# Kernel optimization log

Hardware: AMD Instinct MI355X
Metric: run time of the kernel (lower is better)

Reference implementation:

```python
import jax, jax.numpy as jnp
import numpy as np

B, G, D, L, F = 64, 1024, 256, 2, 1024  # batch, graph_size, embed_dim, n_layers, ffn hidden
NEG = -30.0  # mask fill value when evaluate=False (training path)


def _uniform(key, shape, fan):
    stdv = 1.0 / np.sqrt(fan)
    return jax.random.uniform(key, shape, jnp.float32, -stdv, stdv)


def setup_inputs() -> dict:
    key = jax.random.key(0)
    ks = jax.random.split(key, 12)
    x = jax.random.normal(ks[0], (B, G, D), jnp.float32)
    mask = jax.random.randint(ks[1], (B, G), 0, 2, jnp.int32)  # 1 = attention blocked
    # weights stored as [in, out] (transposed vs torch Linear); same math.
    Wq = _uniform(ks[2], (L, D, D), D)
    Wk = _uniform(ks[3], (L, D, D), D)
    Wv = _uniform(ks[4], (L, D, D), D)
    Wo = _uniform(ks[5], (L, D, D), D)
    bo = _uniform(ks[6], (L, D), D)
    Wf1 = _uniform(ks[7], (L, D, F), D)
    bf1 = _uniform(ks[8], (L, F), F)
    Wf2 = _uniform(ks[9], (L, F, D), F)
    bf2 = _uniform(ks[10], (L, D), D)
    return {"x": x, "mask": mask, "Wq": Wq, "Wk": Wk, "Wv": Wv,
            "Wo": Wo, "bo": bo, "Wf1": Wf1, "bf1": bf1, "Wf2": Wf2, "bf2": bf2}


def reference(x, mask, Wq, Wk, Wv, Wo, bo, Wf1, bf1, Wf2, bf2):
    # GraphAttentionEncoder with n_heads=1 (key_dim = val_dim = embed_dim).
    m = mask.astype(bool)[:, None, :]            # [B,1,G] -> broadcast over query dim
    norm = 1.0 / jnp.sqrt(jnp.asarray(D, x.dtype))
    h = x
    for l in range(L):
        # --- MultiHeadAttention with residual (SkipConnection) ---
        q = h @ Wq[l]                            # [B,G,D]
        k = h @ Wk[l]
        v = h @ Wv[l]
        c = norm * jnp.einsum('bqd,bkd->bqk', q, k)   # [B,G,G]
        c = jnp.where(m, NEG, c)                 # masked fill (-30, evaluate=False)
        a = jax.nn.softmax(c, axis=-1)
        a = jnp.where(m, 0.0, a)                 # post-softmax zeroing of masked weights
        heads = jnp.einsum('bqk,bkd->bqd', a, v)
        h = h + heads @ Wo[l] + bo[l]
        # --- feed-forward with residual (SkipConnection_Linear) ---
        h = h + jax.nn.relu(h @ Wf1[l] + bf1[l]) @ Wf2[l] + bf2[l]
    return h, h.mean(axis=1)
```

## Files before the change

kernel.cpp:

```cpp
#include <hip/hip_runtime.h>
#include <hip/hip_bf16.h>

#define Bdim 64
#define Gdim 1024
#define Ddim 256
#define Fdim 1024

typedef short s8v __attribute__((ext_vector_type(8)));
typedef short s4v __attribute__((ext_vector_type(4)));
typedef float f4v __attribute__((ext_vector_type(4)));

__device__ __forceinline__ float bf2f(short s){
  return __uint_as_float(((unsigned)(unsigned short)s) << 16);
}
__device__ __forceinline__ short f2bf(float f){
  unsigned u = __float_as_uint(f);
  u = u + 0x7fffu + ((u >> 16) & 1u);
  return (short)(u >> 16);
}
__device__ __forceinline__ s8v ld8(const short* p){ return *(const s8v*)p; }

#define MFMA_BF16(a,b,c) __builtin_amdgcn_mfma_f32_16x16x32_bf16((a),(b),(c),0,0,0)

#define GLDS16(gp, lp) __builtin_amdgcn_global_load_lds( \
    (const __attribute__((address_space(1))) void*)(gp), \
    (__attribute__((address_space(3))) void*)(lp), 16, 0, 0)

__global__ __launch_bounds__(256) void detect_dtype(const unsigned* __restrict__ x,
                                                    int* __restrict__ flag){
  __shared__ int cnt[256];
  int c = 0;
  #pragma unroll
  for (int j=0;j<4;j++){
    unsigned u = x[threadIdx.x*4 + j];
    int e = (u >> 7) & 0xFF;
    c += (e >= 100 && e <= 140) ? 1 : 0;
  }
  cnt[threadIdx.x] = c;
  __syncthreads();
  if (threadIdx.x == 0){
    int s = 0;
    for (int i=0;i<256;i++) s += cnt[i];
    flag[0] = (s >= 512) ? 0 : 1;
  }
}

__global__ void diag_ws(void* o, float v, const int* __restrict__ flag){
  if (threadIdx.x == 0){
    if (flag[0]){ ((float*)o)[0] = v; ((float*)o)[16777216] = v; }
    else        { ((short*)o)[0] = f2bf(v); ((short*)o)[16777216] = f2bf(v); }
  }
}

__global__ __launch_bounds__(256) void cast_in(const void* __restrict__ x,
                                               float* __restrict__ h32,
                                               const int* __restrict__ flag){
  size_t i = ((size_t)blockIdx.x * 256 + threadIdx.x) * 8;
  if (flag[0]){
    const float* xf = (const float*)x;
    #pragma unroll
    for (int j=0;j<8;j++) h32[i+j] = xf[i+j];
  } else {
    s8v v = ld8((const short*)x + i);
    #pragma unroll
    for (int j=0;j<8;j++) h32[i+j] = bf2f(v[j]);
  }
}

__global__ __launch_bounds__(256) void transpose_w(const void* __restrict__ src,
                                                   short* __restrict__ dh, int R, int C,
                                                   const int* __restrict__ flag,
                                                   int dzs, int dbase){
  __shared__ short th[32][33];
  int fl = flag[0];
  size_t soff = (size_t)blockIdx.z * R * C;
  size_t doff = (size_t)dbase + (size_t)blockIdx.z * dzs;
  int c0 = blockIdx.x*32, r0 = blockIdx.y*32;
  int tx = threadIdx.x, ty = threadIdx.y;
  #pragma unroll
  for (int i=ty;i<32;i+=8){
    size_t idx = soff + (size_t)(r0+i)*C + (c0+tx);
    float w = fl ? ((const float*)src)[idx] : bf2f(((const short*)src)[idx]);
    th[i][tx] = f2bf(w);
  }
  __syncthreads();
  #pragma unroll
  for (int i=ty;i<32;i+=8)
    dh[doff + (size_t)(c0+i)*R + (r0+tx)] = th[tx][i];
}

__global__ __launch_bounds__(256) void bias_prep(const void* __restrict__ bo,
                                                 const void* __restrict__ bf1,
                                                 const void* __restrict__ bf2,
                                                 float* __restrict__ biasf,
                                                 const int* __restrict__ flag){
  int fl = flag[0];
  int i = blockIdx.x*256 + threadIdx.x;
  const void* src; int idx;
  if (i < 512){ src = bo; idx = i; }
  else if (i < 2560){ src = bf1; idx = i - 512; }
  else { src = bf2; idx = i - 2560; }
  biasf[i] = fl ? ((const float*)src)[idx] : bf2f(((const short*)src)[idx]);
}

template<int AM, int EPI>
__global__ __launch_bounds__(256) void gemm_t(
    const void* __restrict__ Ap, const short* __restrict__ Bh,
    const float* __restrict__ bias, float* __restrict__ hout,
    short* __restrict__ outb, int N, int K, int lda, int ldb, int Mrows)
{
  constexpr int AT = (AM==2) ? 2 : 1;
  __shared__ short As[AT*128*40];
  __shared__ short Bs[128*40];
  short* Asl = As + 128*40;
  const int tid = threadIdx.x;
  const int lane = tid & 63, wave = tid >> 6;
  const int quad = lane >> 4, l16 = lane & 15;
  const int m0 = blockIdx.x * 128, n0 = blockIdx.y * 128;
  const int wr = wave >> 1, wc = wave & 1;
  f4v acc[4][4];
  #pragma unroll
  for (int i=0;i<4;i++)
    #pragma unroll
    for (int j=0;j<4;j++) acc[i][j] = f4v{0.f,0.f,0.f,0.f};

  for (int k0 = 0; k0 < K; k0 += 32){
    __syncthreads();
    #pragma unroll
    for (int i=0;i<2;i++){
      int v = tid + i*256;
      int r = v >> 2, c8 = (v & 3) * 8;
      if (AM == 0){
        *(s8v*)(&As[r*40 + c8]) = ld8((const short*)Ap + (size_t)(m0 + r)*lda + k0 + c8);
      } else {
        const float* af = (const float*)Ap + (size_t)(m0 + r)*lda + k0 + c8;
        float4 f0 = *(const float4*)af;
        float4 f1 = *(const float4*)(af + 4);
        float fv[8] = {f0.x,f0.y,f0.z,f0.w,f1.x,f1.y,f1.z,f1.w};
        s8v hi, lo;
        #pragma unroll
        for (int j=0;j<8;j++) hi[j] = f2bf(fv[j]);
        *(s8v*)(&As[r*40 + c8]) = hi;
        if (AM == 2){
          #pragma unroll
          for (int j=0;j<8;j++) lo[j] = f2bf(fv[j] - bf2f(hi[j]));
          *(s8v*)(&Asl[r*40 + c8]) = lo;
        }
      }
      *(s8v*)(&Bs[r*40 + c8]) = ld8(Bh + (size_t)(n0 + r)*ldb + k0 + c8);
    }
    __syncthreads();
    s8v ah[4], al[4], bh[4];
    #pragma unroll
    for (int t=0;t<4;t++){
      ah[t] = ld8(&As[(wr*64 + t*16 + l16)*40 + quad*8]);
      bh[t] = ld8(&Bs[(wc*64 + t*16 + l16)*40 + quad*8]);
      if (AM == 2) al[t] = ld8(&Asl[(wr*64 + t*16 + l16)*40 + quad*8]);
    }
    #pragma unroll
    for (int ti=0;ti<4;ti++)
      #pragma unroll
      for (int tj=0;tj<4;tj++){
        acc[ti][tj] = MFMA_BF16(ah[ti], bh[tj], acc[ti][tj]);
        if (AM == 2) acc[ti][tj] = MFMA_BF16(al[ti], bh[tj], acc[ti][tj]);
      }
  }
  #pragma unroll
  for (int tj=0;tj<4;tj++){
    int col = n0 + wc*64 + tj*16 + l16;
    float bs = (EPI==1 || EPI==4) ? (bias ? bias[col] : 0.f) : 0.f;
    #pragma unroll
    for (int ti=0;ti<4;ti++){
      #pragma unroll
      for (int r=0;r<4;r++){
        int row = m0 + wr*64 + ti*16 + quad*4 + r;
        float v = acc[ti][tj][r];
        if (EPI == 0){
          outb[(size_t)row * N + col] = f2bf(v);
        } else if (EPI == 1){
          v += bs; v = v > 0.f ? v : 0.f;
          outb[(size_t)row * N + col] = f2bf(v);
        } else if (EPI == 4){
          size_t idx = (size_t)row * N + col;
          hout[idx] += v + bs;
        } else {
          int sec = col >> 8, c = col & 255;
          if (sec == 0)      outb[(size_t)row*256 + c] = f2bf(v);
          else if (sec == 1) (outb + (size_t)Mrows*256)[(size_t)row*256 + c] = f2bf(v);
          else {
            int bb = row >> 10, g = row & 1023;
            (outb + (size_t)2*Mrows*256)[(size_t)bb*262144 + (size_t)c*1024 + g] = f2bf(v);
          }
        }
      }
    }
  }
}

__global__ __launch_bounds__(512, 2) void flash_attn(
    const short* __restrict__ Q, const short* __restrict__ Kmat,
    const short* __restrict__ Vt, const int* __restrict__ mask,
    short* __restrict__ H)
{
  __shared__ short Ks[2][64*256];
  __shared__ short Vs[2][256*64];
  __shared__ short Ps[8][16*72];
  const int tid = threadIdx.x;
  const int lane = tid & 63, wave = tid >> 6;
  const int quad = lane >> 4, l16 = lane & 15;
  const int bid = blockIdx.x;
  const int b  = (bid & 7) + ((bid >> 6) << 3);
  const int qt = (bid >> 3) & 7;
  const short* Qb  = Q    + (size_t)b*Gdim*Ddim;
  const short* Kb  = Kmat + (size_t)b*Gdim*Ddim;
  const short* Vtb = Vt   + (size_t)b*Ddim*Gdim;
  const int qbase = qt*128 + wave*16;

  auto stage = [&](int buf, int k0){
    #pragma unroll
    for (int i=0;i<4;i++){
      int idx = i*512 + tid;
      int r = idx >> 5, g = idx & 31;
      GLDS16(Kb + (size_t)(k0 + r)*Ddim + ((g ^ (r & 7)) << 3), &Ks[buf][idx*8]);
    }
    #pragma unroll
    for (int i=0;i<4;i++){
      int idx = i*512 + tid;
      int d = idx >> 3, g = idx & 7;
      GLDS16(Vtb + (size_t)d*Gdim + k0 + ((g ^ (d & 7)) << 3), &Vs[buf][idx*8]);
    }
  };

  s8v qf[8];
  #pragma unroll
  for (int s=0;s<8;s++)
    qf[s] = ld8(Qb + (size_t)(qbase + l16)*Ddim + s*32 + quad*8);
  float mrow = -1e9f, lsum = 0.f;
  f4v O[16];
  #pragma unroll
  for (int t=0;t<16;t++) O[t] = f4v{0.f,0.f,0.f,0.f};
  short* Pw = Ps[wave];

  stage(0, 0);
  __syncthreads();
  int cur = 0;
  for (int kt=0; kt<16; kt++){
    const int k0 = kt*64;
    if (kt < 15) stage(cur^1, k0 + 64);
    int mv = mask[b*Gdim + k0 + lane];
    f4v sc[4];
    #pragma unroll
    for (int tj=0;tj<4;tj++) sc[tj] = f4v{0.f,0.f,0.f,0.f};
    const short* Kc = &Ks[cur][0];
    __builtin_amdgcn_s_setprio(1);
    #pragma unroll
    for (int st=0; st<8; st++){
      #pragma unroll
      for (int tj=0;tj<4;tj++){
        int row = tj*16 + l16;
        s8v kb = ld8(Kc + row*256 + (((st*4 + quad) ^ (row & 7)) << 3));
        sc[tj] = MFMA_BF16(kb, qf[st], sc[tj]);
      }
    }
    __builtin_amdgcn_s_setprio(0);
    unsigned long long mb = __ballot(mv != 0);
    float pm = -1e9f;
    #pragma unroll
    for (int tj=0;tj<4;tj++){
      unsigned mb4 = (unsigned)(mb >> (tj*16 + quad*4)) & 15u;
      #pragma unroll
      for (int r=0;r<4;r++){
        float v = sc[tj][r] * 0.0625f;
        if ((mb4 >> r) & 1u) v = -30.f;
        sc[tj][r] = v;
        pm = fmaxf(pm, v);
      }
    }
    pm = fmaxf(pm, __shfl_xor(pm, 16));
    pm = fmaxf(pm, __shfl_xor(pm, 32));
    if (!__all(pm <= mrow + 8.f)){
      float mn = fmaxf(mrow, pm);
      float al = __expf(mrow - mn);
      mrow = mn;
      lsum *= al;
      float alr[4];
      #pragma unroll
      for (int r=0;r<4;r++) alr[r] = __shfl(al, quad*4 + r);
      #pragma unroll
      for (int t=0;t<16;t++)
        #pragma unroll
        for (int r=0;r<4;r++) O[t][r] *= alr[r];
    }
    float ps = 0.f;
    #pragma unroll
    for (int tj=0;tj<4;tj++){
      unsigned mb4 = (unsigned)(mb >> (tj*16 + quad*4)) & 15u;
      s4v pk;
      #pragma unroll
      for (int r=0;r<4;r++){
        float e = __expf(sc[tj][r] - mrow);
        ps += e;
        pk[r] = ((mb4 >> r) & 1u) ? (short)0 : f2bf(e);
      }
      *(s4v*)(&Pw[l16*72 + tj*16 + quad*4]) = pk;
    }
    lsum += ps;
    asm volatile("s_waitcnt lgkmcnt(0)" ::: "memory");
    __builtin_amdgcn_sched_barrier(0);
    const short* Vc = &Vs[cur][0];
    __builtin_amdgcn_s_setprio(1);
    #pragma unroll
    for (int st=0; st<2; st++){
      s8v pa = ld8(&Pw[l16*72 + st*32 + quad*8]);
      #pragma unroll
      for (int tt=0; tt<16; tt++){
        int d = tt*16 + l16;
        s8v vb = ld8(Vc + d*64 + (((st*4 + quad) ^ (d & 7)) << 3));
        O[tt] = MFMA_BF16(pa, vb, O[tt]);
      }
    }
    __builtin_amdgcn_s_setprio(0);
    __syncthreads();
    cur ^= 1;
  }
  float s = lsum;
  s += __shfl_xor(s, 16);
  s += __shfl_xor(s, 32);
  float dnr[4];
  #pragma unroll
  for (int r=0;r<4;r++) dnr[r] = fmaxf(__shfl(s, quad*4 + r), 1e-30f);
  #pragma unroll
  for (int t=0;t<16;t++){
    #pragma unroll
    for (int r=0;r<4;r++){
      int row = qbase + quad*4 + r;
      int col = t*16 + l16;
      H[((size_t)b*Gdim + row)*Ddim + col] = f2bf(O[t][r] / dnr[r]);
    }
  }
}

__global__ __launch_bounds__(256) void mean_partial(const float* __restrict__ h32,
                                                    float* __restrict__ part){
  int b = blockIdx.x, c = blockIdx.y, d = threadIdx.x;
  float s = 0.f;
  for (int g = c*64; g < c*64 + 64; g++)
    s += h32[((size_t)b*Gdim + g)*Ddim + d];
  part[(b*16 + c)*Ddim + d] = s;
}
__global__ __launch_bounds__(256) void mean_final_dyn(const float* __restrict__ part,
                                                      void* __restrict__ out,
                                                      const int* __restrict__ flag){
  int i = blockIdx.x*256 + threadIdx.x;
  int b = i >> 8, d = i & 255;
  float s = 0.f;
  #pragma unroll
  for (int c=0;c<16;c++) s += part[(b*16 + c)*Ddim + d];
  s *= (1.f/1024.f);
  if (flag[0]) ((float*)out)[16777216 + i] = s;
  else         ((short*)out)[16777216 + i] = f2bf(s);
}
__global__ __launch_bounds__(256) void store_h(const float* __restrict__ h32,
                                               void* __restrict__ out,
                                               const int* __restrict__ flag){
  size_t i = (size_t)blockIdx.x*256 + threadIdx.x;
  if (flag[0]) ((float*)out)[i] = h32[i];
  else         ((short*)out)[i] = f2bf(h32[i]);
}

extern "C" void kernel_launch(void* const* d_in, const int* in_sizes, int n_in,
                              void* d_out, int out_size, void* d_ws, size_t ws_size,
                              hipStream_t stream)
{
  const void* xs  = d_in[0];
  const int*  mask= (const int*)d_in[1];
  const void* Wq  = d_in[2];
  const void* Wk  = d_in[3];
  const void* Wv  = d_in[4];
  const void* Wo  = d_in[5];
  const void* bo  = d_in[6];
  const void* Wf1 = d_in[7];
  const void* bf1 = d_in[8];
  const void* Wf2 = d_in[9];
  const void* bf2 = d_in[10];

  const size_t W_ALL = 786432 + 262144 + 1048576 + 1048576 + 12288;
  const size_t BASE  = 256 + 67108864;
  int CB;
  if      (ws_size >= BASE + 134217728ull + W_ALL) CB = 64;
  else if (ws_size >= BASE +  67108864ull + W_ALL) CB = 32;
  else if (ws_size >= BASE +  33554432ull + W_ALL) CB = 16;
  else CB = 0;

  char* p = (char*)d_ws;
  int* flag = (int*)p; p += 256;
  detect_dtype<<<1, 256, 0, stream>>>((const unsigned*)xs, flag);
  if (CB == 0){
    diag_ws<<<1, 64, 0, stream>>>(d_out, 2000.f + (float)(ws_size >> 20), flag);
    return;
  }
  const int M = CB * 1024, nch = 64 / CB;
  float* h32 = (float*)p; p += 67108864;
  char* arena = p;        p += (size_t)CB * 2097152;
  short* WqkvT = (short*)p; p += 786432;
  short* WoT   = (short*)p; p += 262144;
  short* Wf1T  = (short*)p; p += 1048576;
  short* Wf2T  = (short*)p; p += 1048576;
  float* biasf = (float*)p; p += 12288;
  float* part  = (float*)arena;

  short* Qc  = (short*)arena;
  short* Kc  = Qc + (size_t)M*256;
  short* Vtc = Qc + (size_t)2*M*256;
  short* Hc  = Qc + (size_t)3*M*256;
  short* Tc  = Qc;

  cast_in<<<8192, 256, 0, stream>>>(xs, h32, flag);
  dim3 tb(32,8);
  transpose_w<<<dim3(8,8,2),  tb, 0, stream>>>(Wq,  WqkvT, 256, 256,  flag, 196608, 0);
  transpose_w<<<dim3(8,8,2),  tb, 0, stream>>>(Wk,  WqkvT, 256, 256,  flag, 196608, 65536);
  transpose_w<<<dim3(8,8,2),  tb, 0, stream>>>(Wv,  WqkvT, 256, 256,  flag, 196608, 131072);
  transpose_w<<<dim3(8,8,2),  tb, 0, stream>>>(Wo,  WoT,   256, 256,  flag, 65536, 0);
  transpose_w<<<dim3(32,8,2), tb, 0, stream>>>(Wf1, Wf1T,  256, 1024, flag, 262144, 0);
  transpose_w<<<dim3(8,32,2), tb, 0, stream>>>(Wf2, Wf2T,  1024, 256, flag, 262144, 0);
  bias_prep<<<12, 256, 0, stream>>>(bo, bf1, bf2, biasf, flag);

  for (int c=0; c<nch; c++){
    float* hc = h32 + (size_t)c*M*256;
    const int* mc = mask + (size_t)c*M;
    for (int l=0; l<2; l++){
      gemm_t<1,5><<<dim3(M/128,6), 256, 0, stream>>>(hc, WqkvT + l*196608, nullptr,
                                                     nullptr, Qc, 768, 256, 256, 256, M);
      flash_attn<<<dim3(8*CB), 512, 0, stream>>>(Qc, Kc, Vtc, mc, Hc);
      gemm_t<0,4><<<dim3(M/128,2), 256, 0, stream>>>(Hc, WoT + l*65536, biasf + l*256,
                                                     hc, nullptr, 256, 256, 256, 256, M);
      gemm_t<2,1><<<dim3(M/128,8), 256, 0, stream>>>(hc, Wf1T + l*262144, biasf + 512 + l*1024,
                                                     nullptr, Tc, 1024, 256, 256, 256, M);
      gemm_t<0,4><<<dim3(M/128,2), 256, 0, stream>>>(Tc, Wf2T + l*262144, biasf + 2560 + l*256,
                                                     hc, nullptr, 256, 1024, 1024, 1024, M);
    }
  }
  mean_partial<<<dim3(64,16), 256, 0, stream>>>(h32, part);
  store_h<<<65536, 256, 0, stream>>>(h32, d_out, flag);
  mean_final_dyn<<<64, 256, 0, stream>>>(part, d_out, flag);
}
```

Before: 1.176 ms.

## Rewrite flash attention with 32x32 MFMA and split-KV waves within block

The attention kernel switches from 16x16x32 to 32x32x16 bf16 MFMA tiles, with each wave now owning 32 query rows. The block's 8 waves split into two KV halves of 512 keys each, processed in 32-key steps. The two partial softmax states are merged at the end through LDS scratch. The aim is fewer LDS fragment loads per FLOP and better MFMA efficiency, at the cost of more registers, a final cross-wave reduction, and shorter K-loop steps with more per-step overhead.

New measurement: 1.283 ms. +9.1%, slower.

```diff
diff --git a/kernel.cpp b/kernel.cpp
--- a/kernel.cpp
+++ b/kernel.cpp
@@ -9,6 +9,7 @@
 typedef short s8v __attribute__((ext_vector_type(8)));
 typedef short s4v __attribute__((ext_vector_type(4)));
 typedef float f4v __attribute__((ext_vector_type(4)));
+typedef float f16f __attribute__((ext_vector_type(16)));
 
 __device__ __forceinline__ float bf2f(short s){
   return __uint_as_float(((unsigned)(unsigned short)s) << 16);
@@ -21,6 +22,7 @@
 __device__ __forceinline__ s8v ld8(const short* p){ return *(const s8v*)p; }
 
 #define MFMA_BF16(a,b,c) __builtin_amdgcn_mfma_f32_16x16x32_bf16((a),(b),(c),0,0,0)
+#define MFMA32(a,b,c)    __builtin_amdgcn_mfma_f32_32x32x16_bf16((a),(b),(c),0,0,0)
 
 #define GLDS16(gp, lp) __builtin_amdgcn_global_load_lds( \
     (const __attribute__((address_space(1))) void*)(gp), \
@@ -202,140 +204,161 @@
     const short* __restrict__ Vt, const int* __restrict__ mask,
     short* __restrict__ H)
 {
-  __shared__ short Ks[2][64*256];
-  __shared__ short Vs[2][256*64];
-  __shared__ short Ps[8][16*72];
+  __shared__ short Ks[2][2][8192];
+  __shared__ short Vs[2][2][8192];
+  __shared__ short Ps[8][1280];
   const int tid = threadIdx.x;
   const int lane = tid & 63, wave = tid >> 6;
-  const int quad = lane >> 4, l16 = lane & 15;
+  const int hi = lane >> 5, l32 = lane & 31;
+  const int g = wave & 3, kvh = wave >> 2;
   const int bid = blockIdx.x;
   const int b  = (bid & 7) + ((bid >> 6) << 3);
   const int qt = (bid >> 3) & 7;
   const short* Qb  = Q    + (size_t)b*Gdim*Ddim;
   const short* Kb  = Kmat + (size_t)b*Gdim*Ddim;
   const short* Vtb = Vt   + (size_t)b*Ddim*Gdim;
-  const int qbase = qt*128 + wave*16;
-
-  auto stage = [&](int buf, int k0){
-    #pragma unroll
-    for (int i=0;i<4;i++){
-      int idx = i*512 + tid;
-      int r = idx >> 5, g = idx & 31;
-      GLDS16(Kb + (size_t)(k0 + r)*Ddim + ((g ^ (r & 7)) << 3), &Ks[buf][idx*8]);
-    }
-    #pragma unroll
-    for (int i=0;i<4;i++){
-      int idx = i*512 + tid;
-      int d = idx >> 3, g = idx & 7;
-      GLDS16(Vtb + (size_t)d*Gdim + k0 + ((g ^ (d & 7)) << 3), &Vs[buf][idx*8]);
+  const int qbase = qt*128 + g*32;
+
+  int kco[2], vco[2], cdst[2];
+  #pragma unroll
+  for (int i=0;i<2;i++){
+    int idx = i*512 + tid;
+    int r = idx >> 5, gg = idx & 31;
+    kco[i] = r*256 + ((gg ^ (r & 7)) << 3);
+    int d = idx >> 2, gv = idx & 3;
+    vco[i] = d*1024 + ((gv ^ (d & 3)) << 3);
+    cdst[i] = idx*8;
+  }
+  auto stage = [&](int buf, int it){
+    const short* k0p = Kb + (size_t)(it*32)*256;
+    const short* k1p = k0p + 512*256;
+    #pragma unroll
+    for (int i=0;i<2;i++){
+      GLDS16(k0p + kco[i], &Ks[0][buf][cdst[i]]);
+      GLDS16(k1p + kco[i], &Ks[1][buf][cdst[i]]);
+      GLDS16(Vtb + vco[i] + it*32,       &Vs[0][buf][cdst[i]]);
+      GLDS16(Vtb + vco[i] + it*32 + 512, &Vs[1][buf][cdst[i]]);
     }
   };
 
-  s8v qf[8];
-  #pragma unroll
-  for (int s=0;s<8;s++)
-    qf[s] = ld8(Qb + (size_t)(qbase + l16)*Ddim + s*32 + quad*8);
+  s8v qf[16];
+  const short* Qrow = Qb + (size_t)(qbase + l32)*Ddim + hi*8;
+  #pragma unroll
+  for (int s=0;s<16;s++) qf[s] = ld8(Qrow + s*16);
   float mrow = -1e9f, lsum = 0.f;
-  f4v O[16];
-  #pragma unroll
-  for (int t=0;t<16;t++) O[t] = f4v{0.f,0.f,0.f,0.f};
+  f16f O[8];
+  #pragma unroll
+  for (int dg=0;dg<8;dg++)
+    #pragma unroll
+    for (int r=0;r<16;r++) O[dg][r] = 0.f;
   short* Pw = Ps[wave];
 
   stage(0, 0);
   __syncthreads();
   int cur = 0;
-  for (int kt=0; kt<16; kt++){
-    const int k0 = kt*64;
-    if (kt < 15) stage(cur^1, k0 + 64);
-    int mv = mask[b*Gdim + k0 + lane];
-    f4v sc[4];
-    #pragma unroll
-    for (int tj=0;tj<4;tj++) sc[tj] = f4v{0.f,0.f,0.f,0.f};
-    const short* Kc = &Ks[cur][0];
+  const short* KsS = &Ks[kvh][0][0];
+  const short* VsS = &Vs[kvh][0][0];
+  const int mbase = b*Gdim + kvh*512;
+  for (int it=0; it<16; it++){
+    if (it < 15) stage(cur^1, it+1);
+    int mv = mask[mbase + it*32 + l32];
+    f16f sc;
+    #pragma unroll
+    for (int r=0;r<16;r++) sc[r] = 0.f;
+    const short* Kst = KsS + cur*8192;
+    const int krow = l32*256, ksw = l32 & 7;
     __builtin_amdgcn_s_setprio(1);
     #pragma unroll
-    for (int st=0; st<8; st++){
-      #pragma unroll
-      for (int tj=0;tj<4;tj++){
-        int row = tj*16 + l16;
-        s8v kb = ld8(Kc + row*256 + (((st*4 + quad) ^ (row & 7)) << 3));
-        sc[tj] = MFMA_BF16(kb, qf[st], sc[tj]);
-      }
+    for (int s=0;s<16;s++){
+      s8v kf = ld8(Kst + krow + (((s*2 + hi) ^ ksw) << 3));
+      sc = MFMA32(kf, qf[s], sc);
     }
     __builtin_amdgcn_s_setprio(0);
-    unsigned long long mb = __ballot(mv != 0);
+    unsigned mb = (unsigned)__ballot(mv != 0);
     float pm = -1e9f;
     #pragma unroll
-    for (int tj=0;tj<4;tj++){
-      unsigned mb4 = (unsigned)(mb >> (tj*16 + quad*4)) & 15u;
-      #pragma unroll
-      for (int r=0;r<4;r++){
-        float v = sc[tj][r] * 0.0625f;
-        if ((mb4 >> r) & 1u) v = -30.f;
-        sc[tj][r] = v;
-        pm = fmaxf(pm, v);
-      }
-    }
-    pm = fmaxf(pm, __shfl_xor(pm, 16));
+    for (int r=0;r<16;r++){
+      int kk = (r & 3) + 8*(r >> 2) + 4*hi;
+      float v = sc[r] * 0.0625f;
+      if ((mb >> kk) & 1u) v = -30.f;
+      sc[r] = v;
+      pm = fmaxf(pm, v);
+    }
     pm = fmaxf(pm, __shfl_xor(pm, 32));
     if (!__all(pm <= mrow + 8.f)){
       float mn = fmaxf(mrow, pm);
       float al = __expf(mrow - mn);
-      mrow = mn;
-      lsum *= al;
-      float alr[4];
-      #pragma unroll
-      for (int r=0;r<4;r++) alr[r] = __shfl(al, quad*4 + r);
-      #pragma unroll
-      for (int t=0;t<16;t++)
+      mrow = mn; lsum *= al;
+      #pragma unroll
+      for (int r=0;r<16;r++){
+        float alr = __shfl(al, (r & 3) + 8*(r >> 2) + 4*hi);
         #pragma unroll
-        for (int r=0;r<4;r++) O[t][r] *= alr[r];
+        for (int dg=0;dg<8;dg++) O[dg][r] *= alr;
+      }
     }
     float ps = 0.f;
     #pragma unroll
-    for (int tj=0;tj<4;tj++){
-      unsigned mb4 = (unsigned)(mb >> (tj*16 + quad*4)) & 15u;
+    for (int rq=0; rq<4; rq++){
       s4v pk;
       #pragma unroll
-      for (int r=0;r<4;r++){
-        float e = __expf(sc[tj][r] - mrow);
+      for (int j=0;j<4;j++){
+        int r = rq*4 + j;
+        int kk = j + 8*rq + 4*hi;
+        float e = __expf(sc[r] - mrow);
         ps += e;
-        pk[r] = ((mb4 >> r) & 1u) ? (short)0 : f2bf(e);
-      }
-      *(s4v*)(&Pw[l16*72 + tj*16 + quad*4]) = pk;
+        pk[j] = ((mb >> kk) & 1u) ? (short)0 : f2bf(e);
+      }
+      *(s4v*)(&Pw[l32*40 + rq*8 + hi*4]) = pk;
     }
     lsum += ps;
     asm volatile("s_waitcnt lgkmcnt(0)" ::: "memory");
     __builtin_amdgcn_sched_barrier(0);
-    const short* Vc = &Vs[cur][0];
+    const short* Vst = VsS + cur*8192;
     __builtin_amdgcn_s_setprio(1);
     #pragma unroll
-    for (int st=0; st<2; st++){
-      s8v pa = ld8(&Pw[l16*72 + st*32 + quad*8]);
-      #pragma unroll
-      for (int tt=0; tt<16; tt++){
-        int d = tt*16 + l16;
-        s8v vb = ld8(Vc + d*64 + (((st*4 + quad) ^ (d & 7)) << 3));
-        O[tt] = MFMA_BF16(pa, vb, O[tt]);
+    for (int c=0;c<2;c++){
+      s8v pa = ld8(&Pw[l32*40 + c*16 + hi*8]);
+      #pragma unroll
+      for (int dg=0;dg<8;dg++){
+        int d = dg*32 + l32;
+        s8v vb = ld8(Vst + d*32 + ((((c*2 + hi) ^ (d & 3))) << 3));
+        O[dg] = MFMA32(pa, vb, O[dg]);
       }
     }
     __builtin_amdgcn_s_setprio(0);
     __syncthreads();
     cur ^= 1;
   }
-  float s = lsum;
-  s += __shfl_xor(s, 16);
-  s += __shfl_xor(s, 32);
-  float dnr[4];
-  #pragma unroll
-  for (int r=0;r<4;r++) dnr[r] = fmaxf(__shfl(s, quad*4 + r), 1e-30f);
-  #pragma unroll
-  for (int t=0;t<16;t++){
-    #pragma unroll
-    for (int r=0;r<4;r++){
-      int row = qbase + quad*4 + r;
-      int col = t*16 + l16;
-      H[((size_t)b*Gdim + row)*Ddim + col] = f2bf(O[t][r] / dnr[r]);
+  float dn = lsum + __shfl_xor(lsum, 32);
+  float* scr = (g < 2) ? ((float*)&Ks[0][0][0] + g*8192)
+                       : ((float*)&Vs[0][0][0] + (g - 2)*8192);
+  float* ml = (float*)&Ps[0][0];
+  if (kvh == 1){
+    #pragma unroll
+    for (int dg=0;dg<8;dg++)
+      #pragma unroll
+      for (int r=0;r<16;r++)
+        scr[(dg*16 + r)*64 + lane] = O[dg][r];
+    if (hi == 0){ ml[g*32 + l32] = mrow; ml[128 + g*32 + l32] = dn; }
+  }
+  __syncthreads();
+  if (kvh == 0){
+    float mh = ml[g*32 + l32], dh = ml[128 + g*32 + l32];
+    float m12 = fmaxf(mrow, mh);
+    float el = __expf(mrow - m12), eh = __expf(mh - m12);
+    float dnf = dn*el + dh*eh;
+    #pragma unroll
+    for (int r=0;r<16;r++){
+      int cr = (r & 3) + 8*(r >> 2) + 4*hi;
+      float elr = __shfl(el, cr);
+      float ehr = __shfl(eh, cr);
+      float dnr = fmaxf(__shfl(dnf, cr), 1e-30f);
+      int row = qbase + cr;
+      #pragma unroll
+      for (int dg=0;dg<8;dg++){
+        float ov = O[dg][r]*elr + scr[(dg*16 + r)*64 + lane]*ehr;
+        H[((size_t)b*Gdim + row)*Ddim + dg*32 + l32] = f2bf(ov / dnr);
+      }
     }
   }
 }
```

## Split KV sequence across wave halves with 32-row query tiles per wave

Applied to the files above, without the earlier changes.

Each wave now handles 32 query rows, so every K and V fragment loaded from LDS feeds two MFMAs instead of one. The eight waves split into two groups that each cover half of the key sequence, in 32-key chunks, and at the end the partial softmax states are merged through shared memory. The aim is to cut LDS read traffic per MFMA and shorten the serial KV loop. In exchange the accumulator register count doubles, which may pressure occupancy at launch bounds (512,2), and a cross-wave merge step is added.

Measured after the change: 1.295 ms. +10.2%, slower.

```diff
diff --git a/kernel.cpp b/kernel.cpp
--- a/kernel.cpp
+++ b/kernel.cpp
@@ -202,140 +202,182 @@
     const short* __restrict__ Vt, const int* __restrict__ mask,
     short* __restrict__ H)
 {
-  __shared__ short Ks[2][64*256];
-  __shared__ short Vs[2][256*64];
-  __shared__ short Ps[8][16*72];
+  __shared__ short Ks[2][2][32*256];
+  __shared__ short Vs[2][2][256*32];
+  __shared__ short Ps[8][32*40];
   const int tid = threadIdx.x;
   const int lane = tid & 63, wave = tid >> 6;
   const int quad = lane >> 4, l16 = lane & 15;
+  const int g = wave & 3, kvh = wave >> 2;
   const int bid = blockIdx.x;
   const int b  = (bid & 7) + ((bid >> 6) << 3);
   const int qt = (bid >> 3) & 7;
   const short* Qb  = Q    + (size_t)b*Gdim*Ddim;
   const short* Kb  = Kmat + (size_t)b*Gdim*Ddim;
   const short* Vtb = Vt   + (size_t)b*Ddim*Gdim;
-  const int qbase = qt*128 + wave*16;
-
-  auto stage = [&](int buf, int k0){
-    #pragma unroll
-    for (int i=0;i<4;i++){
+  const int qbase = qt*128 + g*32;
+
+  auto stage = [&](int buf, int it){
+    #pragma unroll
+    for (int i=0;i<2;i++){
       int idx = i*512 + tid;
-      int r = idx >> 5, g = idx & 31;
-      GLDS16(Kb + (size_t)(k0 + r)*Ddim + ((g ^ (r & 7)) << 3), &Ks[buf][idx*8]);
-    }
-    #pragma unroll
-    for (int i=0;i<4;i++){
-      int idx = i*512 + tid;
-      int d = idx >> 3, g = idx & 7;
-      GLDS16(Vtb + (size_t)d*Gdim + k0 + ((g ^ (d & 7)) << 3), &Vs[buf][idx*8]);
+      int r = idx >> 5, gg = idx & 31;
+      int ko = r*256 + ((gg ^ (r & 7)) << 3);
+      GLDS16(Kb + (size_t)(it*32)*256 + ko,        &Ks[0][buf][idx*8]);
+      GLDS16(Kb + (size_t)(512 + it*32)*256 + ko,  &Ks[1][buf][idx*8]);
+      int d = idx >> 2, gv = idx & 3;
+      int vo = d*1024 + ((gv ^ (d & 3)) << 3);
+      GLDS16(Vtb + vo + it*32,        &Vs[0][buf][idx*8]);
+      GLDS16(Vtb + vo + it*32 + 512,  &Vs[1][buf][idx*8]);
     }
   };
 
-  s8v qf[8];
-  #pragma unroll
-  for (int s=0;s<8;s++)
-    qf[s] = ld8(Qb + (size_t)(qbase + l16)*Ddim + s*32 + quad*8);
-  float mrow = -1e9f, lsum = 0.f;
-  f4v O[16];
-  #pragma unroll
-  for (int t=0;t<16;t++) O[t] = f4v{0.f,0.f,0.f,0.f};
+  s8v qf0[8], qf1[8];
+  {
+    const short* Qr0 = Qb + (size_t)(qbase + l16)*Ddim + quad*8;
+    #pragma unroll
+    for (int s=0;s<8;s++){
+      qf0[s] = ld8(Qr0 + s*32);
+      qf1[s] = ld8(Qr0 + 16*Ddim + s*32);
+    }
+  }
+  float mrow0 = -1e9f, mrow1 = -1e9f, lsum0 = 0.f, lsum1 = 0.f;
+  f4v O0[16], O1[16];
+  #pragma unroll
+  for (int t=0;t<16;t++){ O0[t]=f4v{0.f,0.f,0.f,0.f}; O1[t]=f4v{0.f,0.f,0.f,0.f}; }
   short* Pw = Ps[wave];
+  const int ksw = l16 & 7, vsw = quad ^ (l16 & 3);
 
   stage(0, 0);
   __syncthreads();
   int cur = 0;
-  for (int kt=0; kt<16; kt++){
-    const int k0 = kt*64;
-    if (kt < 15) stage(cur^1, k0 + 64);
-    int mv = mask[b*Gdim + k0 + lane];
-    f4v sc[4];
-    #pragma unroll
-    for (int tj=0;tj<4;tj++) sc[tj] = f4v{0.f,0.f,0.f,0.f};
-    const short* Kc = &Ks[cur][0];
+  const int mbase = b*Gdim + kvh*512;
+  for (int it=0; it<16; it++){
+    if (it < 15) stage(cur^1, it+1);
+    int mv = mask[mbase + it*32 + (lane & 31)];
+    f4v sc0[2], sc1[2];
+    sc0[0]=sc0[1]=f4v{0.f,0.f,0.f,0.f};
+    sc1[0]=sc1[1]=f4v{0.f,0.f,0.f,0.f};
+    const short* Kst = &Ks[kvh][cur][0];
     __builtin_amdgcn_s_setprio(1);
     #pragma unroll
     for (int st=0; st<8; st++){
-      #pragma unroll
-      for (int tj=0;tj<4;tj++){
-        int row = tj*16 + l16;
-        s8v kb = ld8(Kc + row*256 + (((st*4 + quad) ^ (row & 7)) << 3));
-        sc[tj] = MFMA_BF16(kb, qf[st], sc[tj]);
-      }
+      int off = (((st*4 + quad) ^ ksw) << 3);
+      s8v kfa = ld8(Kst + l16*256 + off);
+      s8v kfb = ld8(Kst + (16 + l16)*256 + off);
+      sc0[0] = MFMA_BF16(kfa, qf0[st], sc0[0]);
+      sc0[1] = MFMA_BF16(kfb, qf0[st], sc0[1]);
+      sc1[0] = MFMA_BF16(kfa, qf1[st], sc1[0]);
+      sc1[1] = MFMA_BF16(kfb, qf1[st], sc1[1]);
     }
     __builtin_amdgcn_s_setprio(0);
-    unsigned long long mb = __ballot(mv != 0);
-    float pm = -1e9f;
-    #pragma unroll
-    for (int tj=0;tj<4;tj++){
-      unsigned mb4 = (unsigned)(mb >> (tj*16 + quad*4)) & 15u;
-      #pragma unroll
-      for (int r=0;r<4;r++){
-        float v = sc[tj][r] * 0.0625f;
-        if ((mb4 >> r) & 1u) v = -30.f;
-        sc[tj][r] = v;
-        pm = fmaxf(pm, v);
-      }
-    }
-    pm = fmaxf(pm, __shfl_xor(pm, 16));
-    pm = fmaxf(pm, __shfl_xor(pm, 32));
-    if (!__all(pm <= mrow + 8.f)){
-      float mn = fmaxf(mrow, pm);
-      float al = __expf(mrow - mn);
-      mrow = mn;
-      lsum *= al;
-      float alr[4];
-      #pragma unroll
-      for (int r=0;r<4;r++) alr[r] = __shfl(al, quad*4 + r);
-      #pragma unroll
-      for (int t=0;t<16;t++)
+    unsigned mb = (unsigned)__ballot(mv != 0);
+    auto smax = [&](f4v* sc, float& mr, float& ls, f4v* O, int prow){
+      float pm = -1e9f;
+      #pragma unroll
+      for (int tj=0;tj<2;tj++)
         #pragma unroll
-        for (int r=0;r<4;r++) O[t][r] *= alr[r];
-    }
-    float ps = 0.f;
-    #pragma unroll
-    for (int tj=0;tj<4;tj++){
-      unsigned mb4 = (unsigned)(mb >> (tj*16 + quad*4)) & 15u;
-      s4v pk;
-      #pragma unroll
-      for (int r=0;r<4;r++){
-        float e = __expf(sc[tj][r] - mrow);
-        ps += e;
-        pk[r] = ((mb4 >> r) & 1u) ? (short)0 : f2bf(e);
-      }
-      *(s4v*)(&Pw[l16*72 + tj*16 + quad*4]) = pk;
-    }
-    lsum += ps;
+        for (int r=0;r<4;r++){
+          float v = sc[tj][r] * 0.0625f;
+          if ((mb >> (tj*16 + quad*4 + r)) & 1u) v = -30.f;
+          sc[tj][r] = v;
+          pm = fmaxf(pm, v);
+        }
+      pm = fmaxf(pm, __shfl_xor(pm, 16));
+      pm = fmaxf(pm, __shfl_xor(pm, 32));
+      if (!__all(pm <= mr + 8.f)){
+        float mn = fmaxf(mr, pm);
+        float al = __expf(mr - mn);
+        mr = mn; ls *= al;
+        float alr[4];
+        #pragma unroll
+        for (int r=0;r<4;r++) alr[r] = __shfl(al, quad*4 + r);
+        #pragma unroll
+        for (int t=0;t<16;t++)
+          #pragma unroll
+          for (int r=0;r<4;r++) O[t][r] *= alr[r];
+      }
+      float ps = 0.f;
+      #pragma unroll
+      for (int tj=0;tj<2;tj++){
+        s4v pk;
+        #pragma unroll
+        for (int r=0;r<4;r++){
+          float e = __expf(sc[tj][r] - mr);
+          ps += e;
+          pk[r] = ((mb >> (tj*16 + quad*4 + r)) & 1u) ? (short)0 : f2bf(e);
+        }
+        *(s4v*)(&Pw[(prow + l16)*40 + tj*16 + quad*4]) = pk;
+      }
+      ls += ps;
+    };
+    smax(sc0, mrow0, lsum0, O0, 0);
+    smax(sc1, mrow1, lsum1, O1, 16);
     asm volatile("s_waitcnt lgkmcnt(0)" ::: "memory");
     __builtin_amdgcn_sched_barrier(0);
-    const short* Vc = &Vs[cur][0];
+    const short* Vst = &Vs[kvh][cur][0];
     __builtin_amdgcn_s_setprio(1);
-    #pragma unroll
-    for (int st=0; st<2; st++){
-      s8v pa = ld8(&Pw[l16*72 + st*32 + quad*8]);
-      #pragma unroll
-      for (int tt=0; tt<16; tt++){
-        int d = tt*16 + l16;
-        s8v vb = ld8(Vc + d*64 + (((st*4 + quad) ^ (d & 7)) << 3));
-        O[tt] = MFMA_BF16(pa, vb, O[tt]);
-      }
+    s8v pa0 = ld8(&Pw[l16*40 + quad*8]);
+    s8v pa1 = ld8(&Pw[(16 + l16)*40 + quad*8]);
+    #pragma unroll
+    for (int tt=0; tt<16; tt++){
+      int d = tt*16 + l16;
+      s8v vb = ld8(Vst + d*32 + (vsw << 3));
+      O0[tt] = MFMA_BF16(pa0, vb, O0[tt]);
+      O1[tt] = MFMA_BF16(pa1, vb, O1[tt]);
     }
     __builtin_amdgcn_s_setprio(0);
     __syncthreads();
     cur ^= 1;
   }
-  float s = lsum;
-  s += __shfl_xor(s, 16);
-  s += __shfl_xor(s, 32);
-  float dnr[4];
-  #pragma unroll
-  for (int r=0;r<4;r++) dnr[r] = fmaxf(__shfl(s, quad*4 + r), 1e-30f);
-  #pragma unroll
-  for (int t=0;t<16;t++){
+  float s0 = lsum0; s0 += __shfl_xor(s0, 16); s0 += __shfl_xor(s0, 32);
+  float s1 = lsum1; s1 += __shfl_xor(s1, 16); s1 += __shfl_xor(s1, 32);
+  float* scr = (g < 2) ? ((float*)&Ks[0][0][0] + g*8192)
+                       : ((float*)&Vs[0][0][0] + (g - 2)*8192);
+  float* ml = (float*)&Ps[0][0];
+  if (kvh == 1){
+    #pragma unroll
+    for (int t=0;t<16;t++)
+      #pragma unroll
+      for (int r=0;r<4;r++){
+        scr[(quad*4 + r)*256 + t*16 + l16]        = O0[t][r];
+        scr[(16 + quad*4 + r)*256 + t*16 + l16]   = O1[t][r];
+      }
+    if (quad == 0){
+      ml[g*64 + l16]        = mrow0;  ml[g*64 + 16 + l16]      = mrow1;
+      ml[256 + g*64 + l16]  = s0;     ml[256 + g*64 + 16 + l16] = s1;
+    }
+  }
+  __syncthreads();
+  if (kvh == 0){
+    float mh0 = ml[g*64 + l16],      dh0 = ml[256 + g*64 + l16];
+    float mh1 = ml[g*64 + 16 + l16], dh1 = ml[256 + g*64 + 16 + l16];
+    float m0 = fmaxf(mrow0, mh0), m1 = fmaxf(mrow1, mh1);
+    float el0 = __expf(mrow0 - m0), eh0 = __expf(mh0 - m0);
+    float el1 = __expf(mrow1 - m1), eh1 = __expf(mh1 - m1);
+    float dn0 = fmaxf(s0*el0 + dh0*eh0, 1e-30f);
+    float dn1 = fmaxf(s1*el1 + dh1*eh1, 1e-30f);
+    float el0r[4], eh0r[4], dn0r[4], el1r[4], eh1r[4], dn1r[4];
     #pragma unroll
     for (int r=0;r<4;r++){
-      int row = qbase + quad*4 + r;
-      int col = t*16 + l16;
-      H[((size_t)b*Gdim + row)*Ddim + col] = f2bf(O[t][r] / dnr[r]);
+      int src = quad*4 + r;
+      el0r[r] = __shfl(el0, src); eh0r[r] = __shfl(eh0, src);
+      dn0r[r] = __shfl(dn0, src);
+      el1r[r] = __shfl(el1, src); eh1r[r] = __shfl(eh1, src);
+      dn1r[r] = __shfl(dn1, src);
+    }
+    #pragma unroll
+    for (int t=0;t<16;t++){
+      #pragma unroll
+      for (int r=0;r<4;r++){
+        int col = t*16 + l16;
+        int row0 = qbase + quad*4 + r;
+        float ov0 = O0[t][r]*el0r[r] + scr[(quad*4 + r)*256 + col]*eh0r[r];
+        H[((size_t)b*Gdim + row0)*Ddim + col] = f2bf(ov0 / dn0r[r]);
+        int row1 = qbase + 16 + quad*4 + r;
+        float ov1 = O1[t][r]*el1r[r] + scr[(16 + quad*4 + r)*256 + col]*eh1r[r];
+        H[((size_t)b*Gdim + row1)*Ddim + col] = f2bf(ov1 / dn1r[r]);
+      }
     }
   }
 }
```
